# Kernel optimization log

Hardware: AMD Instinct MI355X
Metric: run time of the kernel (lower is better)

## Reference

```python
import jax, jax.numpy as jnp
import numpy as np

jax.config.update('jax_enable_x64', True)  # 60-bit packed voxel ids need int64

V, H, W, C, P = 8, 128, 128, 512, 128
VOXEL_SIZE = 0.05
NUM_VOXELS = 120000  # target_num_voxels; upper bound on unique voxels here
MAXI = (1 << 20) - 1


def _layernorm(x, g, b, eps=1e-5):
    mu = jnp.mean(x, axis=-1, keepdims=True)
    var = jnp.mean((x - mu) ** 2, axis=-1, keepdims=True)
    return (x - mu) * jax.lax.rsqrt(var + eps) * g + b


def setup_inputs() -> dict:
    key = jax.random.key(0)
    ks = jax.random.split(key, 16)
    features = jax.random.normal(ks[0], (V, H, W, C), jnp.float32)
    depth = jax.random.uniform(ks[1], (V, H, W), jnp.float32, minval=0.2, maxval=1.0)
    K = jnp.broadcast_to(jnp.array([[100.0, 0.0, W / 2.0], [0.0, 100.0, H / 2.0], [0.0, 0.0, 1.0]], jnp.float32), (V, 3, 3))
    R = jnp.broadcast_to(jnp.eye(3, dtype=jnp.float32), (V, 3, 3))
    t = jax.random.uniform(ks[2], (V, 3, 1), jnp.float32, minval=-0.1, maxval=0.1)
    extrinsics = jnp.concatenate([R, t], axis=-1)  # [V,3,4] world->cam
    conf = jax.random.normal(ks[3], (V, H, W), jnp.float32)
    s = 0.02
    return {
        'features': features, 'depth': depth, 'intrinsics': K, 'extrinsics': extrinsics, 'conf': conf,
        'w_proj1': jax.random.normal(ks[4], (C, C), jnp.float32) * s, 'b_proj1': jnp.zeros((C,), jnp.float32),
        'g_ln1': jnp.ones((C,), jnp.float32), 'be_ln1': jnp.zeros((C,), jnp.float32),
        'w_proj2': jax.random.normal(ks[5], (C, C), jnp.float32) * s, 'b_proj2': jnp.zeros((C,), jnp.float32),
        'w_pos1': jax.random.normal(ks[6], (3, P), jnp.float32) * s, 'b_pos1': jnp.zeros((P,), jnp.float32),
        'w_pos2': jax.random.normal(ks[7], (P, P), jnp.float32) * s, 'b_pos2': jnp.zeros((P,), jnp.float32),
        'w_fuse': jax.random.normal(ks[8], (C + P, C), jnp.float32) * s, 'b_fuse': jnp.zeros((C,), jnp.float32),
        'g_ln2': jnp.ones((C,), jnp.float32), 'be_ln2': jnp.zeros((C,), jnp.float32),
    }


def reference(features, depth, intrinsics, extrinsics, conf,
              w_proj1, b_proj1, g_ln1, be_ln1, w_proj2, b_proj2,
              w_pos1, b_pos1, w_pos2, b_pos2, w_fuse, b_fuse, g_ln2, be_ln2):
    # ---- backproject depth to world coords ----
    y, x = jnp.meshgrid(jnp.arange(H, dtype=depth.dtype), jnp.arange(W, dtype=depth.dtype), indexing='ij')
    pixels = jnp.stack([x, y, jnp.ones_like(x)], axis=-1).reshape(H * W, 3)  # [HW,3]
    Kinv = jnp.linalg.inv(intrinsics)                                        # [V,3,3]
    cam = jnp.einsum('vij,pj->vpi', Kinv, pixels) * depth.reshape(V, H * W, 1)
    cam_h = jnp.concatenate([cam, jnp.ones((V, H * W, 1), cam.dtype)], axis=-1)
    bottom = jnp.broadcast_to(jnp.array([[0.0, 0.0, 0.0, 1.0]], extrinsics.dtype), (V, 1, 4))
    E4 = jnp.concatenate([extrinsics, bottom], axis=1)                       # world->cam 4x4
    Einv = jnp.linalg.inv(E4)                                                # cam->world
    world = jnp.einsum('vij,vpj->vpi', Einv[:, :3, :], cam_h)                # [V,HW,3]
    pts = world.reshape(-1, 3)                                               # [N,3]

    # ---- voxel indices + packed 60-bit voxel id ----
    vox = pts / VOXEL_SIZE
    idx = jnp.round(vox).astype(jnp.int64)
    ix = jnp.clip(idx[:, 0], 0, MAXI)
    iy = jnp.clip(idx[:, 1], 0, MAXI)
    iz = jnp.clip(idx[:, 2], 0, MAXI)
    vid = (ix << 40) | (iy << 20) | iz                                       # [N]

    # ---- group points by voxel id (static-size unique -> segment ids) ----
    u_ids, seg = jnp.unique(vid, size=NUM_VOXELS, fill_value=-1, return_inverse=True)
    seg = seg.reshape(-1)

    # ---- per-voxel softmax pooling weights (scatter_max + scatter_add) ----
    scores = jax.nn.softplus(conf.reshape(-1))
    m = jax.ops.segment_max(scores, seg, num_segments=NUM_VOXELS)
    e = jnp.exp(scores - m[seg])
    denom = jax.ops.segment_sum(e, seg, num_segments=NUM_VOXELS)
    wgt = e / jnp.maximum(denom[seg], 1e-12)

    # ---- weighted scatter-add of features ----
    feats = features.reshape(-1, C)
    vfeat = jax.ops.segment_sum(feats * wgt[:, None], seg, num_segments=NUM_VOXELS)  # [S,C]

    # ---- voxel centers decoded from packed id ----
    cxi = (u_ids >> 40) & MAXI
    cyi = (u_ids >> 20) & MAXI
    czi = u_ids & MAXI
    valid = (u_ids >= 0)
    centers = jnp.stack([cxi, cyi, czi], axis=-1).astype(vfeat.dtype) * VOXEL_SIZE
    centers = jnp.where(valid[:, None], centers, 0.0)

    # ---- voxel_feat_proj: Linear -> LN -> GELU -> Linear ----
    h = vfeat @ w_proj1 + b_proj1
    h = jax.nn.gelu(_layernorm(h, g_ln1, be_ln1), approximate=False)
    h = h @ w_proj2 + b_proj2

    # ---- pos_encoding: Linear -> SiLU -> Linear ----
    pe = jax.nn.silu(centers @ w_pos1 + b_pos1) @ w_pos2 + b_pos2

    # ---- token_fusion: Linear -> LN -> GELU ----
    tok = jnp.concatenate([h, pe], axis=-1) @ w_fuse + b_fuse
    tok = jax.nn.gelu(_layernorm(tok, g_ln2, be_ln2), approximate=False)
    return tok * valid[:, None].astype(tok.dtype)
```

## Files before the change

### kernel.cpp

```cpp
#include <hip/hip_runtime.h>
#include <hip/hip_bf16.h>
#include <math.h>

#define V 8
#define H 128
#define W 128
#define C 512
#define P 128
#define HW (H*W)
#define NPTS (V*HW)
#define MAXI ((1<<20)-1)
#define ROWCAP 8192
#define PROWCAP 5376
#define NROWS 120000
#define DGRID 65536
#define PERM(d) ((((d) & 15) << 12) | ((d) >> 4))
#define NCH 5

#define SCAT_BLOCKS 1024
#define WT_BLOCKS   832
#define POS_BLOCKS  (ROWCAP/8)
#define MEGA_BLOCKS (SCAT_BLOCKS + WT_BLOCKS + POS_BLOCKS)

#define PZB 512
#define GZB 512

typedef __attribute__((ext_vector_type(8))) short short8v;
typedef __attribute__((ext_vector_type(4))) float f32x4;

__device__ __forceinline__ float softplusf(float x){
  return fmaxf(x, 0.0f) + log1pf(expf(-fabsf(x)));
}
__device__ __forceinline__ float geluf(float x){
  return 0.5f * x * (1.0f + erff(x * 0.70710678118654752440f));
}
__device__ __forceinline__ short f2bf_s(float x){
  __hip_bfloat16 h = __float2bfloat16(x);
  return *(short*)&h;
}

__device__ __forceinline__ void zero_chunk(float* __restrict__ outp, int chunk,
                                           int nblocks, int blk, int tid){
  f32x4* out4 = (f32x4*)outp;
  size_t start = (size_t)PROWCAP * 128;
  size_t total = (size_t)NROWS * 128;
  size_t n = total - start;
  size_t per = (n + NCH - 1) / NCH;
  size_t cs = start + (size_t)chunk * per;
  size_t ce = cs + per; if (ce > total) ce = total;
  size_t stride = (size_t)nblocks * 256;
  f32x4 z = (f32x4){0.f,0.f,0.f,0.f};
  for (size_t i = cs + (size_t)blk*256 + tid; i < ce; i += stride)
    __builtin_nontemporal_store(z, &out4[i]);
}

__device__ void wT_tile(const float* __restrict__ w, __hip_bfloat16* __restrict__ wT,
                        int K, int bx, int by){
  __shared__ float tile[32][33];
  int kb = bx*32, nb = by*32;
  int tx = threadIdx.x & 31, ty = threadIdx.x >> 5;
  for (int i = ty; i < 32; i += 8){
    int k = kb + i;
    tile[i][tx] = (k < K) ? w[(size_t)k*512 + nb + tx] : 0.f;
  }
  __syncthreads();
  for (int i = ty; i < 32; i += 8){
    int n = nb + i;
    int k = kb + tx;
    if (k < K) wT[(size_t)n*K + k] = __float2bfloat16(tile[tx][i]);
  }
}

__global__ __launch_bounds__(256) void k_points(const float* __restrict__ depth,
    const float* __restrict__ Kmat, const float* __restrict__ Emat,
    int* __restrict__ scnt, unsigned short* __restrict__ didp, int* __restrict__ witp,
    float* __restrict__ outp){
  int blk = blockIdx.x;
  int tid = threadIdx.x;
  if (blk >= NPTS/256){ zero_chunk(outp, 0, PZB, blk - NPTS/256, tid); return; }
  int p = blk*256 + tid;
  int v = blk >> 6;
  const float* K = Kmat + v*9;
  float a=K[0],b=K[1],c=K[2],d=K[3],e=K[4],f=K[5],g=K[6],h=K[7],i=K[8];
  float det = a*(e*i-f*h) - b*(d*i-f*g) + c*(d*h-e*g);
  float kin = 1.0f/det;
  float k0=(e*i-f*h)*kin, k1=(c*h-b*i)*kin, k2=(b*f-c*e)*kin;
  float k3=(f*g-d*i)*kin, k4=(a*i-c*g)*kin, k5=(c*d-a*f)*kin;
  float k6=(d*h-e*g)*kin, k7=(b*g-a*h)*kin, k8=(a*e-b*d)*kin;
  const float* E = Emat + v*12;
  float r00=E[0],r01=E[1],r02=E[2],t0=E[3];
  float r10=E[4],r11=E[5],r12=E[6],t1=E[7];
  float r20=E[8],r21=E[9],r22=E[10],t2=E[11];
  float rdet = r00*(r11*r22-r12*r21) - r01*(r10*r22-r12*r20) + r02*(r10*r21-r11*r20);
  float rinv = 1.0f/rdet;
  float i00=(r11*r22-r12*r21)*rinv, i01=(r02*r21-r01*r22)*rinv, i02=(r01*r12-r02*r11)*rinv;
  float i10=(r12*r20-r10*r22)*rinv, i11=(r00*r22-r02*r20)*rinv, i12=(r02*r10-r00*r12)*rinv;
  float i20=(r10*r21-r11*r20)*rinv, i21=(r01*r20-r00*r21)*rinv, i22=(r00*r11-r01*r10)*rinv;
  float j0=-(i00*t0+i01*t1+i02*t2), j1=-(i10*t0+i11*t1+i12*t2), j2=-(i20*t0+i21*t1+i22*t2);

  int pix = p & (HW-1);
  float fx = (float)(pix & 127);
  float fy = (float)(pix >> 7);
  float dep = depth[p];
  float cx = (k0*fx + k1*fy + k2) * dep;
  float cy = (k3*fx + k4*fy + k5) * dep;
  float cz = (k6*fx + k7*fy + k8) * dep;
  float wx = i00*cx + i01*cy + i02*cz + j0;
  float wy = i10*cx + i11*cy + i12*cz + j1;
  float wz = i20*cx + i21*cy + i22*cz + j2;
  long long ix = (long long)rintf(wx / 0.05f);
  long long iy = (long long)rintf(wy / 0.05f);
  long long iz = (long long)rintf(wz / 0.05f);
  ix = ix < 0 ? 0 : (ix > MAXI ? (long long)MAXI : ix);
  iy = iy < 0 ? 0 : (iy > MAXI ? (long long)MAXI : iy);
  iz = iz < 0 ? 0 : (iz > MAXI ? (long long)MAXI : iz);
  int dx = (int)(ix > 31 ? 31 : ix);
  int dy = (int)(iy > 31 ? 31 : iy);
  int dz = (int)(iz > 63 ? 63 : iz);
  int did = (dx << 11) | (dy << 6) | dz;
  didp[p] = (unsigned short)did;
  witp[p] = atomicAdd(&scnt[PERM(did)], 1);
}

__global__ __launch_bounds__(256) void k_scan1(const int* __restrict__ scnt,
    int* __restrict__ exwb, int* __restrict__ bsum){
  int tid = threadIdx.x;
  int did = blockIdx.x*256 + tid;
  int cnt = scnt[PERM(did)];
  int vpk = (cnt << 13) | (cnt > 0);
  int lane = tid & 63, wv = tid >> 6;
  int s = vpk;
  #pragma unroll
  for (int off = 1; off < 64; off <<= 1){
    int t = __shfl_up(s, off);
    if (lane >= off) s += t;
  }
  __shared__ int wsum[4];
  if (lane == 63) wsum[wv] = s;
  __syncthreads();
  int woff = 0;
  #pragma unroll
  for (int k = 0; k < 4; k++) woff += (k < wv) ? wsum[k] : 0;
  int incl = s + woff;
  exwb[did] = incl - vpk;
  if (tid == 255) bsum[blockIdx.x] = incl;
}

__global__ __launch_bounds__(256) void k_scan2(const int* __restrict__ scnt,
    const int* __restrict__ exwb, const int* __restrict__ bsum,
    int* __restrict__ row_of_dense, int* __restrict__ ustart_dense,
    int* __restrict__ dense_of_row, int* __restrict__ Sc){
  int tid = threadIdx.x, b = blockIdx.x;
  int lane = tid & 63, wv = tid >> 6;
  int vsum = (tid < b) ? bsum[tid] : 0;
  #pragma unroll
  for (int off = 32; off; off >>= 1) vsum += __shfl_down(vsum, off);
  __shared__ int rsum[4];
  if (lane == 0) rsum[wv] = vsum;
  __syncthreads();
  int prefix = rsum[0] + rsum[1] + rsum[2] + rsum[3];
  int did = b*256 + tid;
  int cnt = scnt[PERM(did)];
  int excl = exwb[did] + prefix;
  ustart_dense[did] = excl >> 13;
  int row = excl & 8191;
  row_of_dense[did] = row;
  if (cnt > 0) dense_of_row[row] = did;
  if (b == 255 && tid == 255)
    *Sc = (excl + ((cnt << 13) | (cnt > 0))) & 8191;
}

__global__ __launch_bounds__(256) void k_fill(const unsigned short* __restrict__ didp,
    const int* __restrict__ witp, const int* __restrict__ row_of_dense,
    const int* __restrict__ ustart_dense, const float* __restrict__ conf,
    int* __restrict__ pcsr, int* __restrict__ rcsr, float* __restrict__ wcsr){
  int p = blockIdx.x*256 + threadIdx.x;
  int did = didp[p];
  int idx = ustart_dense[did] + witp[p];
  pcsr[idx] = p;
  rcsr[idx] = row_of_dense[did];
  wcsr[idx] = expf(softplusf(conf[p]));
}

__global__ __launch_bounds__(256) void k_mega(
    const float* __restrict__ feats,
    const int* __restrict__ pcsr, const int* __restrict__ rcsr, const float* __restrict__ wcsr,
    float* __restrict__ vraw, float* __restrict__ esum,
    const int* __restrict__ Sc, const int* __restrict__ dense_of_row,
    const float* __restrict__ wp1, const float* __restrict__ bp1,
    const float* __restrict__ wp2, const float* __restrict__ bp2,
    __hip_bfloat16* __restrict__ pebf,
    const float* __restrict__ w1, __hip_bfloat16* __restrict__ w1T,
    const float* __restrict__ w2, __hip_bfloat16* __restrict__ w2T,
    const float* __restrict__ wf, __hip_bfloat16* __restrict__ wfT){
  int blk = blockIdx.x;
  int tid = threadIdx.x;

  if (blk < SCAT_BLOCKS){
    __shared__ int pp[4][32];
    __shared__ int rr[4][32];
    __shared__ float ww[4][32];
    if (tid < 128){
      int e = blk*128 + tid;
      pp[tid>>5][tid&31] = pcsr[e];
      rr[tid>>5][tid&31] = rcsr[e];
      ww[tid>>5][tid&31] = wcsr[e];
    }
    __syncthreads();
    int q = tid >> 6, ln = tid & 63;
    f32x4 accA0 = (f32x4){0.f,0.f,0.f,0.f};
    f32x4 accA1 = (f32x4){0.f,0.f,0.f,0.f};
    float eA = 0.f;
    int curA = rr[q][0];
    f32x4 accP0 = (f32x4){0.f,0.f,0.f,0.f};
    f32x4 accP1 = (f32x4){0.f,0.f,0.f,0.f};
    float eP = 0.f;
    int curP = -1;
    #define FLUSH(row_, x0_, x1_, e_) { \
      float* vp = &vraw[(size_t)(row_)*C + ln*4]; \
      atomicAdd(vp+0, (x0_)[0]); atomicAdd(vp+1, (x0_)[1]); \
      atomicAdd(vp+2, (x0_)[2]); atomicAdd(vp+3, (x0_)[3]); \
      float* vq = vp + 256; \
      atomicAdd(vq+0, (x1_)[0]); atomicAdd(vq+1, (x1_)[1]); \
      atomicAdd(vq+2, (x1_)[2]); atomicAdd(vq+3, (x1_)[3]); \
      if (ln == 0) atomicAdd(&esum[row_], (e_)); }
    for (int i = 0; i < 32; i += 8){
      f32x4 a0,a1,a2,a3,a4,a5,a6,a7, b0,b1,b2,b3,b4,b5,b6,b7;
      {
        const float* f0 = feats + (size_t)pp[q][i+0]*C + ln*4;
        const float* f1 = feats + (size_t)pp[q][i+1]*C + ln*4;
        const float* f2 = feats + (size_t)pp[q][i+2]*C + ln*4;
        const float* f3 = feats + (size_t)pp[q][i+3]*C + ln*4;
        const float* f4 = feats + (size_t)pp[q][i+4]*C + ln*4;
        const float* f5 = feats + (size_t)pp[q][i+5]*C + ln*4;
        const float* f6 = feats + (size_t)pp[q][i+6]*C + ln*4;
        const float* f7 = feats + (size_t)pp[q][i+7]*C + ln*4;
        a0 = *(const f32x4*)f0; b0 = *(const f32x4*)(f0 + 256);
        a1 = *(const f32x4*)f1; b1 = *(const f32x4*)(f1 + 256);
        a2 = *(const f32x4*)f2; b2 = *(const f32x4*)(f2 + 256);
        a3 = *(const f32x4*)f3; b3 = *(const f32x4*)(f3 + 256);
        a4 = *(const f32x4*)f4; b4 = *(const f32x4*)(f4 + 256);
        a5 = *(const f32x4*)f5; b5 = *(const f32x4*)(f5 + 256);
        a6 = *(const f32x4*)f6; b6 = *(const f32x4*)(f6 + 256);
        a7 = *(const f32x4*)f7; b7 = *(const f32x4*)(f7 + 256);
      }
      #define STEP(u, av, bv) { \
        int r_ = rr[q][i+u]; float w_ = ww[q][i+u]; \
        if (r_ != curA){ \
          if (curP >= 0){ FLUSH(curP, accP0, accP1, eP); } \
          curP = curA; accP0 = accA0; accP1 = accA1; eP = eA; \
          curA = r_; \
          accA0 = (f32x4){0.f,0.f,0.f,0.f}; accA1 = (f32x4){0.f,0.f,0.f,0.f}; eA = 0.f; \
        } \
        accA0 += av * w_; accA1 += bv * w_; eA += w_; }
      STEP(0, a0, b0) STEP(1, a1, b1) STEP(2, a2, b2) STEP(3, a3, b3)
      STEP(4, a4, b4) STEP(5, a5, b5) STEP(6, a6, b6) STEP(7, a7, b7)
      #undef STEP
    }
    if (curP >= 0){ FLUSH(curP, accP0, accP1, eP); }
    FLUSH(curA, accA0, accA1, eA);
    #undef FLUSH
    return;
  }
  blk -= SCAT_BLOCKS;

  if (blk < WT_BLOCKS){
    if (blk < 256)      wT_tile(w1, w1T, 512, blk & 15, blk >> 4);
    else if (blk < 512){ int t = blk - 256; wT_tile(w2, w2T, 512, t & 15, t >> 4); }
    else               { int t = blk - 512; wT_tile(wf, wfT, 640, t % 20, t / 20); }
    return;
  }
  blk -= WT_BLOCKS;

  {
    int S = *Sc; if (S > ROWCAP) S = ROWCAP;
    int r0 = blk * 8;
    if (r0 >= S) return;
    __shared__ float t1[8][128];
    __shared__ float cen[8][4];
    if (tid < 8){
      int r = r0 + tid;
      int d = (r < S) ? dense_of_row[r] : 0;
      cen[tid][0] = (float)(d >> 11) * 0.05f;
      cen[tid][1] = (float)((d >> 6) & 31) * 0.05f;
      cen[tid][2] = (float)(d & 63) * 0.05f;
    }
    __syncthreads();
    #pragma unroll
    for (int it = 0; it < 4; it++){
      int idx = tid + it*256;
      int r = idx >> 7, j = idx & 127;
      float a = cen[r][0]*wp1[j] + cen[r][1]*wp1[P + j] + cen[r][2]*wp1[2*P + j] + bp1[j];
      t1[r][j] = a / (1.0f + expf(-a));
    }
    __syncthreads();
    #pragma unroll
    for (int it = 0; it < 4; it++){
      int idx = tid + it*256;
      int r = idx >> 7, j = idx & 127;
      if (r0 + r < S){
        float acc = bp2[j];
        for (int k = 0; k < P; k++) acc = fmaf(t1[r][k], wp2[k*P + j], acc);
        pebf[(size_t)(r0+r)*P + j] = __float2bfloat16(acc);
      }
    }
  }
}

__global__ __launch_bounds__(256) void k_gemm1(const float* __restrict__ vraw,
    const float* __restrict__ esum, const __hip_bfloat16* __restrict__ Bt,
    const float* __restrict__ bias, float* __restrict__ Cout, const int* __restrict__ Sc,
    float* __restrict__ outz){
  int blk = blockIdx.x;
  int tid = threadIdx.x;
  if (blk >= 1024){ zero_chunk(outz, 1, GZB, blk - 1024, tid); return; }
  int S = *Sc; if (S > ROWCAP) S = ROWCAP;
  int m0 = (blk >> 3) * 64;
  if (m0 >= S) return;
  int n0 = (blk & 7) * 64;
  __shared__ short As[64][40];
  __shared__ short Bs[64][40];
  int l = tid & 63, w = tid >> 6;
  int wr = w >> 1, wc = w & 1;
  f32x4 acc[2][2];
  #pragma unroll
  for (int i=0;i<2;i++)
    #pragma unroll
    for (int j=0;j<2;j++) acc[i][j] = (f32x4){0.f,0.f,0.f,0.f};

  int arow = tid >> 2, akq = tid & 3;
  int gm = m0 + arow;
  float inv = 0.f;
  if (gm < S) inv = 1.0f / fmaxf(esum[gm], 1e-12f);
  for (int kb = 0; kb < 512; kb += 32){
    {
      int kg = kb + akq*8;
      short8v av = (short8v){0,0,0,0,0,0,0,0};
      if (gm < S){
        f32x4 va = *(const f32x4*)(vraw + (size_t)gm*512 + kg);
        f32x4 vb = *(const f32x4*)(vraw + (size_t)gm*512 + kg + 4);
        av[0]=f2bf_s(va[0]*inv); av[1]=f2bf_s(va[1]*inv);
        av[2]=f2bf_s(va[2]*inv); av[3]=f2bf_s(va[3]*inv);
        av[4]=f2bf_s(vb[0]*inv); av[5]=f2bf_s(vb[1]*inv);
        av[6]=f2bf_s(vb[2]*inv); av[7]=f2bf_s(vb[3]*inv);
      }
      *(short8v*)&As[arow][akq*8] = av;
      short8v bv = *(const short8v*)(Bt + (size_t)(n0 + arow)*512 + kb + akq*8);
      *(short8v*)&Bs[arow][akq*8] = bv;
    }
    __syncthreads();
    short8v a0 = *(const short8v*)&As[wr*32 + (l & 15)][(l >> 4)*8];
    short8v a1 = *(const short8v*)&As[wr*32 + 16 + (l & 15)][(l >> 4)*8];
    short8v b0 = *(const short8v*)&Bs[wc*32 + (l & 15)][(l >> 4)*8];
    short8v b1 = *(const short8v*)&Bs[wc*32 + 16 + (l & 15)][(l >> 4)*8];
    acc[0][0] = __builtin_amdgcn_mfma_f32_16x16x32_bf16(a0, b0, acc[0][0], 0, 0, 0);
    acc[0][1] = __builtin_amdgcn_mfma_f32_16x16x32_bf16(a0, b1, acc[0][1], 0, 0, 0);
    acc[1][0] = __builtin_amdgcn_mfma_f32_16x16x32_bf16(a1, b0, acc[1][0], 0, 0, 0);
    acc[1][1] = __builtin_amdgcn_mfma_f32_16x16x32_bf16(a1, b1, acc[1][1], 0, 0, 0);
    __syncthreads();
  }
  float bias0 = bias[n0 + wc*32 +  0 + (l & 15)];
  float bias1 = bias[n0 + wc*32 + 16 + (l & 15)];
  #pragma unroll
  for (int i = 0; i < 2; i++){
    #pragma unroll
    for (int j = 0; j < 2; j++){
      int n = n0 + wc*32 + j*16 + (l & 15);
      float bj = j ? bias1 : bias0;
      #pragma unroll
      for (int r = 0; r < 4; r++){
        int m = m0 + wr*32 + i*16 + (l >> 4)*4 + r;
        if (m < S) Cout[(size_t)m*512 + n] = acc[i][j][r] + bj;
      }
    }
  }
}

template<int OUTBF, int CHUNK>
__global__ __launch_bounds__(256) void k_gemm_mfma(
    const __hip_bfloat16* __restrict__ A1, int lda1, int K1,
    const __hip_bfloat16* __restrict__ A2, int lda2,
    const __hip_bfloat16* __restrict__ Bt, int ldb,
    const float* __restrict__ bias, void* __restrict__ Cout,
    int Kdim, const int* __restrict__ Sc, float* __restrict__ outz){
  int blk = blockIdx.x;
  int tid = threadIdx.x;
  if (blk >= 1024){ zero_chunk(outz, CHUNK, GZB, blk - 1024, tid); return; }
  int S = *Sc; if (S > ROWCAP) S = ROWCAP;
  int m0 = (blk >> 3) * 64;
  if (m0 >= S) return;
  int n0 = (blk & 7) * 64;
  __shared__ short As[64][40];
  __shared__ short Bs[64][40];
  int l = tid & 63, w = tid >> 6;
  int wr = w >> 1, wc = w & 1;
  f32x4 acc[2][2];
  #pragma unroll
  for (int i=0;i<2;i++)
    #pragma unroll
    for (int j=0;j<2;j++) acc[i][j] = (f32x4){0.f,0.f,0.f,0.f};

  int arow = tid >> 2, akq = tid & 3;
  for (int kb = 0; kb < Kdim; kb += 32){
    {
      int kg = kb + akq*8;
      short8v av = (short8v){0,0,0,0,0,0,0,0};
      int gm = m0 + arow;
      if (gm < S){
        const __hip_bfloat16* src = (kg < K1) ? (A1 + (size_t)gm*lda1 + kg)
                                              : (A2 + (size_t)gm*lda2 + (kg - K1));
        av = *(const short8v*)src;
      }
      *(short8v*)&As[arow][akq*8] = av;
      short8v bv = *(const short8v*)(Bt + (size_t)(n0 + arow)*ldb + kb + akq*8);
      *(short8v*)&Bs[arow][akq*8] = bv;
    }
    __syncthreads();
    short8v a0 = *(const short8v*)&As[wr*32 + (l & 15)][(l >> 4)*8];
    short8v a1 = *(const short8v*)&As[wr*32 + 16 + (l & 15)][(l >> 4)*8];
    short8v b0 = *(const short8v*)&Bs[wc*32 + (l & 15)][(l >> 4)*8];
    short8v b1 = *(const short8v*)&Bs[wc*32 + 16 + (l & 15)][(l >> 4)*8];
    acc[0][0] = __builtin_amdgcn_mfma_f32_16x16x32_bf16(a0, b0, acc[0][0], 0, 0, 0);
    acc[0][1] = __builtin_amdgcn_mfma_f32_16x16x32_bf16(a0, b1, acc[0][1], 0, 0, 0);
    acc[1][0] = __builtin_amdgcn_mfma_f32_16x16x32_bf16(a1, b0, acc[1][0], 0, 0, 0);
    acc[1][1] = __builtin_amdgcn_mfma_f32_16x16x32_bf16(a1, b1, acc[1][1], 0, 0, 0);
    __syncthreads();
  }
  float bias0 = bias[n0 + wc*32 +  0 + (l & 15)];
  float bias1 = bias[n0 + wc*32 + 16 + (l & 15)];
  #pragma unroll
  for (int i = 0; i < 2; i++){
    #pragma unroll
    for (int j = 0; j < 2; j++){
      int n = n0 + wc*32 + j*16 + (l & 15);
      float bj = j ? bias1 : bias0;
      #pragma unroll
      for (int r = 0; r < 4; r++){
        int m = m0 + wr*32 + i*16 + (l >> 4)*4 + r;
        if (m < S){
          float val = acc[i][j][r] + bj;
          if (OUTBF) ((__hip_bfloat16*)Cout)[(size_t)m*512 + n] = __float2bfloat16(val);
          else       ((float*)Cout)[(size_t)m*512 + n] = val;
        }
      }
    }
  }
}

__global__ __launch_bounds__(256) void k_ln_gelu(const float* __restrict__ in,
    __hip_bfloat16* __restrict__ outp, const float* __restrict__ g, const float* __restrict__ b,
    const int* __restrict__ Sc, float* __restrict__ outz){
  int tid = threadIdx.x;
  if (blockIdx.x >= 2048){ zero_chunk(outz, 2, GZB, blockIdx.x - 2048, tid); return; }
  int S = *Sc; if (S > ROWCAP) S = ROWCAP;
  __shared__ float red[8];
  int lane = tid & 63, wid = tid >> 6;
  for (int row = blockIdx.x; row < S; row += 2048){
    float x0 = in[(size_t)row*C + tid];
    float x1 = in[(size_t)row*C + tid + 256];
    float s = x0 + x1;
    for (int o_=32;o_;o_>>=1) s += __shfl_down(s, o_);
    if (lane == 0) red[wid] = s;
    __syncthreads();
    float mu = (red[0]+red[1]+red[2]+red[3]) * (1.0f/C);
    __syncthreads();
    float d0 = x0-mu, d1 = x1-mu;
    float q = d0*d0 + d1*d1;
    for (int o_=32;o_;o_>>=1) q += __shfl_down(q, o_);
    if (lane == 0) red[wid] = q;
    __syncthreads();
    float var = (red[0]+red[1]+red[2]+red[3]) * (1.0f/C);
    float rs = rsqrtf(var + 1e-5f);
    float y0 = d0*rs*g[tid]     + b[tid];
    float y1 = d1*rs*g[tid+256] + b[tid+256];
    outp[(size_t)row*C + tid]       = __float2bfloat16(geluf(y0));
    outp[(size_t)row*C + tid + 256] = __float2bfloat16(geluf(y1));
    __syncthreads();
  }
}

__global__ __launch_bounds__(256) void k_ln_gelu_out(const float* __restrict__ in,
    float* __restrict__ outp, const float* __restrict__ g, const float* __restrict__ b,
    const int* __restrict__ Sc){
  int S = *Sc; if (S > ROWCAP) S = ROWCAP;
  __shared__ float red[8];
  int tid = threadIdx.x;
  int lane = tid & 63, wid = tid >> 6;
  for (int row = blockIdx.x; row < S; row += gridDim.x){
    float x0 = in[(size_t)row*C + tid];
    float x1 = in[(size_t)row*C + tid + 256];
    float s = x0 + x1;
    for (int o_=32;o_;o_>>=1) s += __shfl_down(s, o_);
    if (lane == 0) red[wid] = s;
    __syncthreads();
    float mu = (red[0]+red[1]+red[2]+red[3]) * (1.0f/C);
    __syncthreads();
    float d0 = x0-mu, d1 = x1-mu;
    float q = d0*d0 + d1*d1;
    for (int o_=32;o_;o_>>=1) q += __shfl_down(q, o_);
    if (lane == 0) red[wid] = q;
    __syncthreads();
    float var = (red[0]+red[1]+red[2]+red[3]) * (1.0f/C);
    float rs = rsqrtf(var + 1e-5f);
    float y0 = d0*rs*g[tid]     + b[tid];
    float y1 = d1*rs*g[tid+256] + b[tid+256];
    __builtin_nontemporal_store(geluf(y0), &outp[(size_t)row*C + tid]);
    __builtin_nontemporal_store(geluf(y1), &outp[(size_t)row*C + tid + 256]);
    __syncthreads();
  }
  for (int row = S + blockIdx.x; row < PROWCAP; row += gridDim.x){
    __builtin_nontemporal_store(0.f, &outp[(size_t)row*C + tid]);
    __builtin_nontemporal_store(0.f, &outp[(size_t)row*C + tid + 256]);
  }
}

extern "C" void kernel_launch(void* const* d_in, const int* in_sizes, int n_in,
                              void* d_out, int out_size, void* d_ws, size_t ws_size,
                              hipStream_t stream){
  const float* features = (const float*)d_in[0];
  const float* depth    = (const float*)d_in[1];
  const float* intr     = (const float*)d_in[2];
  const float* extr     = (const float*)d_in[3];
  const float* conf     = (const float*)d_in[4];
  const float* w1  = (const float*)d_in[5];
  const float* b1  = (const float*)d_in[6];
  const float* g1  = (const float*)d_in[7];
  const float* be1 = (const float*)d_in[8];
  const float* w2  = (const float*)d_in[9];
  const float* b2  = (const float*)d_in[10];
  const float* wp1 = (const float*)d_in[11];
  const float* bp1 = (const float*)d_in[12];
  const float* wp2 = (const float*)d_in[13];
  const float* bp2 = (const float*)d_in[14];
  const float* wf  = (const float*)d_in[15];
  const float* bf  = (const float*)d_in[16];
  const float* g2  = (const float*)d_in[17];
  const float* be2 = (const float*)d_in[18];

  char* ws = (char*)d_ws;
  size_t o = 0;
  auto alloc = [&](size_t bytes){ void* p = ws + o; o += (bytes + 255) & ~size_t(255); return p; };
  int*   scnt    = (int*)alloc((size_t)DGRID*4);
  int*   Sc      = (int*)alloc(256);
  float* esum    = (float*)alloc((size_t)ROWCAP*4);
  float* vraw    = (float*)alloc((size_t)ROWCAP*C*4);
  size_t zspan = (size_t)((char*)vraw + (size_t)ROWCAP*C*4 - (char*)scnt);
  unsigned short* didp = (unsigned short*)alloc((size_t)NPTS*2);
  int*   witp    = (int*)alloc((size_t)NPTS*4);
  int*   pcsr    = (int*)alloc((size_t)NPTS*4);
  int*   rcsr    = (int*)alloc((size_t)NPTS*4);
  float* wcsr    = (float*)alloc((size_t)NPTS*4);
  int*   exwb    = (int*)alloc((size_t)DGRID*4);
  int*   bsum    = (int*)alloc(256*4);
  int*   row_of_dense   = (int*)alloc((size_t)DGRID*4);
  int*   ustart_dense   = (int*)alloc((size_t)DGRID*4);
  int*   dense_of_row   = (int*)alloc((size_t)ROWCAP*4);
  float*          hbufA = (float*)alloc((size_t)ROWCAP*C*4);
  __hip_bfloat16* h1bf = (__hip_bfloat16*)alloc((size_t)ROWCAP*C*2);
  __hip_bfloat16* h2bf = (__hip_bfloat16*)alloc((size_t)ROWCAP*C*2);
  __hip_bfloat16* pebf = (__hip_bfloat16*)alloc((size_t)ROWCAP*P*2);
  __hip_bfloat16* w1T  = (__hip_bfloat16*)alloc((size_t)512*512*2);
  __hip_bfloat16* w2T  = (__hip_bfloat16*)alloc((size_t)512*512*2);
  __hip_bfloat16* wfT  = (__hip_bfloat16*)alloc((size_t)512*640*2);

  float* outp = (float*)d_out;

  hipMemsetAsync(scnt, 0, zspan, stream);

  k_points<<<NPTS/256 + PZB, 256, 0, stream>>>(depth, intr, extr, scnt, didp, witp, outp);
  k_scan1<<<DGRID/256, 256, 0, stream>>>(scnt, exwb, bsum);
  k_scan2<<<DGRID/256, 256, 0, stream>>>(scnt, exwb, bsum, row_of_dense, ustart_dense,
                                         dense_of_row, Sc);
  k_fill<<<NPTS/256, 256, 0, stream>>>(didp, witp, row_of_dense, ustart_dense, conf,
                                       pcsr, rcsr, wcsr);
  k_mega<<<MEGA_BLOCKS, 256, 0, stream>>>(features, pcsr, rcsr, wcsr, vraw, esum,
                                          Sc, dense_of_row,
                                          wp1, bp1, wp2, bp2, pebf,
                                          w1, w1T, w2, w2T, wf, wfT);

  k_gemm1<<<1024 + GZB, 256, 0, stream>>>(vraw, esum, w1T, b1, hbufA, Sc, outp);
  k_ln_gelu<<<2048 + GZB, 256, 0, stream>>>(hbufA, h1bf, g1, be1, Sc, outp);
  k_gemm_mfma<1,3><<<1024 + GZB, 256, 0, stream>>>(h1bf, 512, 512, h1bf, 512, w2T, 512,
                                                   b2, h2bf, 512, Sc, outp);
  k_gemm_mfma<0,4><<<1024 + GZB, 256, 0, stream>>>(h2bf, 512, 512, pebf, 128, wfT, 640,
                                                   bf, hbufA, 640, Sc, outp);
  k_ln_gelu_out<<<2048, 256, 0, stream>>>(hbufA, outp, g2, be2, Sc);
}
```

Before: 238.1 us.

## Split voxel histogram atomics across 32 sub-histograms to cut contention

Points now increment one of 32 per-segment count arrays, picked by point index, instead of a single dense histogram. This spreads atomic contention on hot voxels, which matters because few voxels are occupied. A scan kernel combines the segments into totals and per-segment prefix offsets, and the fill kernel adds those offsets to compute CSR positions. The cost is a 32x larger zeroed count buffer (8 MB memset), 32 strided loads per cell in scan1, and an extra 8 MB segpre write and read.

```diff
diff --git a/kernel.cpp b/kernel.cpp
--- a/kernel.cpp
+++ b/kernel.cpp
@@ -15,6 +15,7 @@
 #define NROWS 120000
 #define DGRID 65536
 #define PERM(d) ((((d) & 15) << 12) | ((d) >> 4))
+#define NSEG 32
 #define NCH 5
 
 #define SCAT_BLOCKS 1024
@@ -119,14 +120,24 @@
   int dz = (int)(iz > 63 ? 63 : iz);
   int did = (dx << 11) | (dy << 6) | dz;
   didp[p] = (unsigned short)did;
-  witp[p] = atomicAdd(&scnt[PERM(did)], 1);
+  int seg = p & (NSEG-1);
+  witp[p] = atomicAdd(&scnt[seg*DGRID + PERM(did)], 1);
 }
 
 __global__ __launch_bounds__(256) void k_scan1(const int* __restrict__ scnt,
+    int* __restrict__ segpre, int* __restrict__ cnt_total,
     int* __restrict__ exwb, int* __restrict__ bsum){
   int tid = threadIdx.x;
   int did = blockIdx.x*256 + tid;
-  int cnt = scnt[PERM(did)];
+  int pj = PERM(did);
+  int c[NSEG];
+  #pragma unroll
+  for (int s = 0; s < NSEG; s++) c[s] = scnt[s*DGRID + pj];
+  int run = 0;
+  #pragma unroll
+  for (int s = 0; s < NSEG; s++){ segpre[(size_t)did*NSEG + s] = run; run += c[s]; }
+  cnt_total[did] = run;
+  int cnt = run;
   int vpk = (cnt << 13) | (cnt > 0);
   int lane = tid & 63, wv = tid >> 6;
   int s = vpk;
@@ -146,7 +157,7 @@
   if (tid == 255) bsum[blockIdx.x] = incl;
 }
 
-__global__ __launch_bounds__(256) void k_scan2(const int* __restrict__ scnt,
+__global__ __launch_bounds__(256) void k_scan2(const int* __restrict__ cnt_total,
     const int* __restrict__ exwb, const int* __restrict__ bsum,
     int* __restrict__ row_of_dense, int* __restrict__ ustart_dense,
     int* __restrict__ dense_of_row, int* __restrict__ Sc){
@@ -160,7 +171,7 @@
   __syncthreads();
   int prefix = rsum[0] + rsum[1] + rsum[2] + rsum[3];
   int did = b*256 + tid;
-  int cnt = scnt[PERM(did)];
+  int cnt = cnt_total[did];
   int excl = exwb[did] + prefix;
   ustart_dense[did] = excl >> 13;
   int row = excl & 8191;
@@ -172,11 +183,13 @@
 
 __global__ __launch_bounds__(256) void k_fill(const unsigned short* __restrict__ didp,
     const int* __restrict__ witp, const int* __restrict__ row_of_dense,
-    const int* __restrict__ ustart_dense, const float* __restrict__ conf,
+    const int* __restrict__ ustart_dense, const int* __restrict__ segpre,
+    const float* __restrict__ conf,
     int* __restrict__ pcsr, int* __restrict__ rcsr, float* __restrict__ wcsr){
   int p = blockIdx.x*256 + threadIdx.x;
   int did = didp[p];
-  int idx = ustart_dense[did] + witp[p];
+  int seg = p & (NSEG-1);
+  int idx = ustart_dense[did] + segpre[(size_t)did*NSEG + seg] + witp[p];
   pcsr[idx] = p;
   rcsr[idx] = row_of_dense[did];
   wcsr[idx] = expf(softplusf(conf[p]));
@@ -540,7 +553,7 @@
   char* ws = (char*)d_ws;
   size_t o = 0;
   auto alloc = [&](size_t bytes){ void* p = ws + o; o += (bytes + 255) & ~size_t(255); return p; };
-  int*   scnt    = (int*)alloc((size_t)DGRID*4);
+  int*   scnt    = (int*)alloc((size_t)NSEG*DGRID*4);
   int*   Sc      = (int*)alloc(256);
   float* esum    = (float*)alloc((size_t)ROWCAP*4);
   float* vraw    = (float*)alloc((size_t)ROWCAP*C*4);
@@ -550,6 +563,8 @@
   int*   pcsr    = (int*)alloc((size_t)NPTS*4);
   int*   rcsr    = (int*)alloc((size_t)NPTS*4);
   float* wcsr    = (float*)alloc((size_t)NPTS*4);
+  int*   segpre  = (int*)alloc((size_t)DGRID*NSEG*4);
+  int*   cnt_total = (int*)alloc((size_t)DGRID*4);
   int*   exwb    = (int*)alloc((size_t)DGRID*4);
   int*   bsum    = (int*)alloc(256*4);
   int*   row_of_dense   = (int*)alloc((size_t)DGRID*4);
@@ -568,10 +583,10 @@
   hipMemsetAsync(scnt, 0, zspan, stream);
 
   k_points<<<NPTS/256 + PZB, 256, 0, stream>>>(depth, intr, extr, scnt, didp, witp, outp);
-  k_scan1<<<DGRID/256, 256, 0, stream>>>(scnt, exwb, bsum);
-  k_scan2<<<DGRID/256, 256, 0, stream>>>(scnt, exwb, bsum, row_of_dense, ustart_dense,
+  k_scan1<<<DGRID/256, 256, 0, stream>>>(scnt, segpre, cnt_total, exwb, bsum);
+  k_scan2<<<DGRID/256, 256, 0, stream>>>(cnt_total, exwb, bsum, row_of_dense, ustart_dense,
                                          dense_of_row, Sc);
-  k_fill<<<NPTS/256, 256, 0, stream>>>(didp, witp, row_of_dense, ustart_dense, conf,
+  k_fill<<<NPTS/256, 256, 0, stream>>>(didp, witp, row_of_dense, ustart_dense, segpre, conf,
                                        pcsr, rcsr, wcsr);
   k_mega<<<MEGA_BLOCKS, 256, 0, stream>>>(features, pcsr, rcsr, wcsr, vraw, esum,
                                           Sc, dense_of_row,
```

Result: faster. 200.6 us, median of 2 (-15.8%).
